# Kernel tuning notes

Hardware: AMD Instinct MI355X
Metric: run time of the kernel (lower is better)

The kernel has to match this reference:

```python
import jax, jax.numpy as jnp
import numpy as np

N_HEAD = 12
MIN_SIZE = 4
MAX_SIZE = 8
TOP_M = 16
ALPHA = 1.0
EPS = 1e-6
NEG_INF = -1e30


def setup_inputs() -> dict:
    key = jax.random.key(0)
    ks = jax.random.split(key, 4)
    B, T, C = 2, 512, 768
    x = jax.random.normal(ks[0], (B, T, C), jnp.float32)
    w_qkv = jax.random.normal(ks[1], (C, 3 * C), jnp.float32) * (1.0 / np.sqrt(C))
    b_qkv = jnp.zeros((3 * C,), jnp.float32)
    w_proj = jax.random.normal(ks[2], (C, C), jnp.float32) * (1.0 / np.sqrt(C))
    b_proj = jnp.zeros((C,), jnp.float32)
    gate_param = jnp.zeros((), jnp.float32)  # dpp_gate_init = 0.0 -> gate = 0.5
    return {"x": x, "w_qkv": w_qkv, "b_qkv": b_qkv, "w_proj": w_proj,
            "b_proj": b_proj, "gate_param": gate_param}


def _dpp_token(i, q_i, k, v):
    """Greedy DPP subset selection + attention for one query token.
    q_i: [hd], k/v: [T, hd]. Faithful to the torch greedy loop, vectorized
    over candidates with incremental Gram construction (scores only gate the
    discrete selection, so they are computed under stop_gradient, matching
    torch where they only feed Python comparisons)."""
    T, hd = k.shape
    kc = jax.lax.stop_gradient(k)
    qc = jax.lax.stop_gradient(q_i)
    # causal similarity, topk candidates
    sim = jnp.where(jnp.arange(T) <= i, kc @ qc, NEG_INF)
    _, topidx = jax.lax.top_k(sim, TOP_M)  # [M]
    # candidates = top-min(TOP_M, i+1) causal neighbors, excluding i itself
    cand_active = (jnp.arange(TOP_M) < jnp.minimum(TOP_M, i + 1)) & (topidx != i)
    cand_keys = kc[topidx]                              # [M, hd]
    cnorm = jnp.sum(cand_keys * cand_keys, axis=-1)     # [M]

    sel_idx = jnp.zeros((MAX_SIZE,), jnp.int32).at[0].set(i)
    sel_count = jnp.int32(1)
    # initial score: log(det([k_i.k_i]) + eps) / 1**alpha
    cur = jnp.log(jnp.dot(kc[i], kc[i]) + EPS)
    stopped = jnp.bool_(False)
    eye = jnp.eye(MAX_SIZE, dtype=jnp.float32)
    slots = jnp.arange(MAX_SIZE)

    for _ in range(MAX_SIZE - 1):
        rowmask = slots < sel_count                       # [S] current subset rows
        pos = (slots == sel_count).astype(jnp.float32)    # slot for new candidate
        Ksel = kc[sel_idx] * rowmask[:, None].astype(jnp.float32)  # [S, hd]
        G0 = Ksel @ Ksel.T                                # [S, S]
        cross = cand_keys @ Ksel.T                        # [M, S]
        # Gc[c,a,b] = G0[a,b] + pos[a]*cross[c,b] + pos[b]*cross[c,a] + pos[a]pos[b]*cnorm[c]
        Gc = (G0[None]
              + pos[None, :, None] * cross[:, None, :]
              + pos[None, None, :] * cross[:, :, None]
              + (pos[:, None] * pos[None, :])[None] * cnorm[:, None, None])
        newmask = rowmask | (slots == sel_count)
        # identity-pad unused rows/cols so det equals det of the active submatrix
        Gc = Gc + (eye * (1.0 - newmask.astype(jnp.float32)))[None]
        dets = jnp.linalg.det(Gc)                         # [M] (float32, as torch)
        size = (sel_count + 1).astype(jnp.float32)
        score = jnp.log(dets + EPS) / size ** ALPHA       # minimize_det=False
        masked = jnp.where(cand_active, score, NEG_INF)
        best = jnp.argmax(masked)
        best_score = masked[best]
        any_cand = jnp.any(cand_active)
        take = any_cand & (~stopped) & ((best_score > cur) | (sel_count < MIN_SIZE))
        sel_idx = jnp.where(take, sel_idx.at[sel_count].set(topidx[best].astype(jnp.int32)), sel_idx)
        cand_active = jnp.where(take, cand_active.at[best].set(False), cand_active)
        cur = jnp.where(take, best_score, cur)
        sel_count = sel_count + take.astype(jnp.int32)
        stopped = stopped | (~take)

    # attention over the selected subset (gradients flow through k, v, q here)
    rowmask = slots < sel_count
    Ks = k[sel_idx]
    Vs = v[sel_idx]
    logits = jnp.where(rowmask, (Ks @ q_i) / np.float32(np.sqrt(hd)), NEG_INF)
    w = jax.nn.softmax(logits)
    return w @ Vs


def _forward(x, w_qkv, b_qkv, w_proj, b_proj, gate_param):
    B, T, C = x.shape
    hd = C // N_HEAD
    qkv = x @ w_qkv + b_qkv
    q, k, v = jnp.split(qkv, 3, axis=-1)

    def heads(t):  # [B,T,C] -> [B*NH, T, hd]
        return t.reshape(B, T, N_HEAD, hd).transpose(0, 2, 1, 3).reshape(B * N_HEAD, T, hd)

    q, k, v = heads(q), heads(k), heads(v)

    # standard causal softmax attention (flash path, dropout=0 at eval)
    scale = np.float32(1.0 / np.sqrt(hd))
    att = jnp.einsum('nqd,nkd->nqk', q, k) * scale
    causal = jnp.tril(jnp.ones((T, T), bool))
    att = jnp.where(causal[None], att, NEG_INF)
    y_std = jnp.einsum('nqk,nkd->nqd', jax.nn.softmax(att, axis=-1), v)

    # DPP greedy-selection attention, vmapped over tokens and (batch*head)
    dpp_head = jax.vmap(_dpp_token, in_axes=(0, 0, None, None))
    y_dpp = jax.vmap(lambda qh, kh, vh: dpp_head(jnp.arange(T), qh, kh, vh))(q, k, v)

    gate = jax.nn.sigmoid(gate_param)
    y = gate * y_dpp + (1.0 - gate) * y_std
    y = y.reshape(B, N_HEAD, T, hd).transpose(0, 2, 1, 3).reshape(B, T, C)
    return y @ w_proj + b_proj


def reference(x, w_qkv, b_qkv, w_proj, b_proj, gate_param):
    return _forward(x, w_qkv, b_qkv, w_proj, b_proj, gate_param)
```

## Files before the change

kernel.cpp:

```cpp
#include <hip/hip_runtime.h>
#include <math.h>

constexpr int SEQ   = 512;
constexpr int HDIM  = 64;
constexpr int NHEAD = 12;
constexpr int NBATCH = 2;
constexpr int CDIM  = 768;
constexpr int TOPM  = 16;
constexpr int SMAX  = 8;
constexpr float NEGINF = -1e30f;

typedef short bf16x8 __attribute__((ext_vector_type(8)));
typedef float f32x4  __attribute__((ext_vector_type(4)));

__device__ inline void gload_lds16(const void* src, void* lds_base)
{
    __builtin_amdgcn_global_load_lds(
        (const __attribute__((address_space(1))) void*)src,
        (__attribute__((address_space(3))) void*)lds_base, 16, 0, 0);
}

__device__ inline unsigned short f2bf(float f)
{
    unsigned u = __float_as_uint(f);
    return (unsigned short)((u + 0x7FFFu + ((u >> 16) & 1u)) >> 16);
}
__device__ inline float bf2f(unsigned short h)
{
    return __uint_as_float((unsigned)h << 16);
}

__global__ __launch_bounds__(256) void split_x_kernel(
    const float* __restrict__ x, unsigned short* __restrict__ xh,
    unsigned short* __restrict__ xm, unsigned short* __restrict__ xl)
{
    const int idx = (blockIdx.x * 256 + threadIdx.x) * 4;
    float4 v = *(const float4*)(x + idx);
    float vv[4] = {v.x, v.y, v.z, v.w};
    unsigned short h[4], m[4], l[4];
    #pragma unroll
    for (int e = 0; e < 4; ++e) {
        float f = vv[e];
        unsigned short bh = f2bf(f);
        float r1 = f - bf2f(bh);
        unsigned short bm2 = f2bf(r1);
        float r2 = r1 - bf2f(bm2);
        h[e] = bh; m[e] = bm2; l[e] = f2bf(r2);
    }
    *(ushort4*)(xh + idx) = make_ushort4(h[0], h[1], h[2], h[3]);
    *(ushort4*)(xm + idx) = make_ushort4(m[0], m[1], m[2], m[3]);
    *(ushort4*)(xl + idx) = make_ushort4(l[0], l[1], l[2], l[3]);
}

__global__ __launch_bounds__(256) void tsplit_w_kernel(
    const float* __restrict__ w, unsigned short* __restrict__ wh,
    unsigned short* __restrict__ wm, unsigned short* __restrict__ wl)
{
    __shared__ float T[64][65];
    const int c0 = blockIdx.x * 64;
    const int k0 = blockIdx.y * 64;
    const int tid = threadIdx.x;
    #pragma unroll
    for (int i = 0; i < 16; ++i) {
        int idx = tid + i * 256;
        int kk = idx >> 6, cc = idx & 63;
        T[kk][cc] = w[(size_t)(k0 + kk) * (3 * CDIM) + c0 + cc];
    }
    __syncthreads();
    #pragma unroll
    for (int i = 0; i < 16; ++i) {
        int idx = tid + i * 256;
        int col = idx >> 6, kk = idx & 63;
        float f = T[kk][col];
        unsigned short bh = f2bf(f);
        float r1 = f - bf2f(bh);
        unsigned short bm2 = f2bf(r1);
        float r2 = r1 - bf2f(bm2);
        size_t o = (size_t)(c0 + col) * CDIM + k0 + kk;
        wh[o] = bh; wm[o] = bm2; wl[o] = f2bf(r2);
    }
}

__global__ __launch_bounds__(256) void qkv_mfma_kernel(
    const unsigned short* __restrict__ xh, const unsigned short* __restrict__ xm,
    const unsigned short* __restrict__ xl, const unsigned short* __restrict__ wh,
    const unsigned short* __restrict__ wm, const unsigned short* __restrict__ wl,
    const float* __restrict__ bias,
    float* __restrict__ q, float* __restrict__ k, float* __restrict__ v)
{
    __shared__ unsigned short As[3][64 * 32];
    __shared__ unsigned short Bs[3][64 * 32];
    const int bn = blockIdx.x * 64;
    const int bm = blockIdx.y * 64;
    const int tid = threadIdx.x;
    const int wid = tid >> 6;
    const int lane = tid & 63;
    const int lrow = lane & 15;
    const int lk8 = (lane >> 4) << 3;

    f32x4 acc[4];
    #pragma unroll
    for (int b = 0; b < 4; ++b) acc[b] = (f32x4){0.f, 0.f, 0.f, 0.f};

    const unsigned short* xs[3] = {xh, xm, xl};
    const unsigned short* wsrc[3] = {wh, wm, wl};

    const int slot = wid * 64 + lane;
    const int srow = slot >> 2;
    const int sk8 = (slot & 3) << 3;

    for (int k0 = 0; k0 < CDIM; k0 += 32) {
        #pragma unroll
        for (int c = 0; c < 3; ++c)
            gload_lds16(xs[c] + (size_t)(bm + srow) * CDIM + k0 + sk8,
                        &As[c][wid * 512]);
        #pragma unroll
        for (int c = 0; c < 3; ++c)
            gload_lds16(wsrc[c] + (size_t)(bn + srow) * CDIM + k0 + sk8,
                        &Bs[c][wid * 512]);
        __syncthreads();

        bf16x8 bf[3][4];
        #pragma unroll
        for (int c = 0; c < 3; ++c)
            #pragma unroll
            for (int ni = 0; ni < 4; ++ni)
                bf[c][ni] = *(const bf16x8*)&Bs[c][(ni * 16 + lrow) * 32 + lk8];

        bf16x8 ah = *(const bf16x8*)&As[0][(wid * 16 + lrow) * 32 + lk8];
        bf16x8 am = *(const bf16x8*)&As[1][(wid * 16 + lrow) * 32 + lk8];
        bf16x8 al = *(const bf16x8*)&As[2][(wid * 16 + lrow) * 32 + lk8];
        #pragma unroll
        for (int ni = 0; ni < 4; ++ni) {
            f32x4 a = acc[ni];
            a = __builtin_amdgcn_mfma_f32_16x16x32_bf16(al, bf[0][ni], a, 0, 0, 0);
            a = __builtin_amdgcn_mfma_f32_16x16x32_bf16(ah, bf[2][ni], a, 0, 0, 0);
            a = __builtin_amdgcn_mfma_f32_16x16x32_bf16(am, bf[1][ni], a, 0, 0, 0);
            a = __builtin_amdgcn_mfma_f32_16x16x32_bf16(am, bf[0][ni], a, 0, 0, 0);
            a = __builtin_amdgcn_mfma_f32_16x16x32_bf16(ah, bf[1][ni], a, 0, 0, 0);
            a = __builtin_amdgcn_mfma_f32_16x16x32_bf16(ah, bf[0][ni], a, 0, 0, 0);
            acc[ni] = a;
        }
        __syncthreads();
    }

    const int rbase = (lane >> 4) << 2;
    #pragma unroll
    for (int ni = 0; ni < 4; ++ni) {
        int cc = bn + ni * 16 + lrow;
        float bval = bias[cc];
        int part = cc / CDIM;
        int c2 = cc - part * CDIM;
        int hh = c2 >> 6, d = c2 & 63;
        float* dst = (part == 0) ? q : ((part == 1) ? k : v);
        #pragma unroll
        for (int r = 0; r < 4; ++r) {
            int m = bm + wid * 16 + rbase + r;
            int b_ = m >> 9, t = m & 511;
            dst[((((size_t)b_ * NHEAD + hh) * SEQ) + t) * HDIM + d] =
                acc[ni][r] + bval;
        }
    }
}

__global__ __launch_bounds__(256) void qkkt_kernel(
    const float* __restrict__ q, const float* __restrict__ k,
    float* __restrict__ S, float* __restrict__ KKT)
{
    __shared__ float Qs[64][68];
    __shared__ float Ka[64][68];
    __shared__ float Kb[64][68];
    const int e = blockIdx.x;
    const int n = blockIdx.y;
    int it = 0, start = 0;
    while (start + it + 1 <= e) { start += it + 1; ++it; }
    const int jt = e - start;
    const int tid = threadIdx.x;
    const float* qh = q + (size_t)n * SEQ * HDIM;
    const float* kh = k + (size_t)n * SEQ * HDIM;

    #pragma unroll
    for (int l = 0; l < 4; ++l) {
        int idx = tid + l * 256;
        int tok = idx >> 4, d4 = (idx & 15) << 2;
        *(float4*)&Qs[tok][d4] = *(const float4*)(qh + (it * 64 + tok) * HDIM + d4);
        *(float4*)&Ka[tok][d4] = *(const float4*)(kh + (it * 64 + tok) * HDIM + d4);
        *(float4*)&Kb[tok][d4] = *(const float4*)(kh + (jt * 64 + tok) * HDIM + d4);
    }
    __syncthreads();

    const int tm = (tid >> 4) << 2;
    const int tn = (tid & 15) << 2;
    float sacc[4][4] = {};
    float gacc[4][4] = {};
    #pragma unroll 4
    for (int d4 = 0; d4 < 16; ++d4) {
        float4 qr[4], ar[4], br[4];
        #pragma unroll
        for (int u = 0; u < 4; ++u) {
            qr[u] = *(const float4*)&Qs[tm + u][d4 << 2];
            ar[u] = *(const float4*)&Ka[tm + u][d4 << 2];
        }
        #pragma unroll
        for (int w2 = 0; w2 < 4; ++w2)
            br[w2] = *(const float4*)&Kb[tn + w2][d4 << 2];
        #pragma unroll
        for (int u = 0; u < 4; ++u)
            #pragma unroll
            for (int w2 = 0; w2 < 4; ++w2) {
                float s = sacc[u][w2];
                s = fmaf(qr[u].x, br[w2].x, s);
                s = fmaf(qr[u].y, br[w2].y, s);
                s = fmaf(qr[u].z, br[w2].z, s);
                s = fmaf(qr[u].w, br[w2].w, s);
                sacc[u][w2] = s;
                float g = gacc[u][w2];
                g = fmaf(ar[u].x, br[w2].x, g);
                g = fmaf(ar[u].y, br[w2].y, g);
                g = fmaf(ar[u].z, br[w2].z, g);
                g = fmaf(ar[u].w, br[w2].w, g);
                gacc[u][w2] = g;
            }
    }
    float* gdst = KKT + ((size_t)n * 36 + e) * 4096;
    #pragma unroll
    for (int u = 0; u < 4; ++u) {
        int i = it * 64 + tm + u;
        float4 o = {sacc[u][0], sacc[u][1], sacc[u][2], sacc[u][3]};
        *(float4*)(S + ((size_t)n * SEQ + i) * SEQ + jt * 64 + tn) = o;
        float4 g = {gacc[u][0], gacc[u][1], gacc[u][2], gacc[u][3]};
        *(float4*)(gdst + (tm + u) * 64 + tn) = g;
    }
}

__device__ inline double hybrid_log(double a)
{
    unsigned long long b = __double_as_longlong(a);
    int e2 = (int)((b >> 52) & 0x7FF) - 1022;
    double m = __longlong_as_double((b & 0x000FFFFFFFFFFFFFULL) |
                                    0x3FE0000000000000ULL);
    return ((double)__log2f((float)m) + (double)e2) * 0.6931471805599453;
}

__device__ inline double rsqrt64(double x)
{
    double r = (double)rsqrtf((float)x);
    r = r * (1.5 - 0.5 * x * r * r);
    return r;
}

#define CSW(a, b)                                                        \
    {                                                                    \
        bool sw = (v##a < v##b) || ((v##a == v##b) && (j##a > j##b));    \
        float tf = sw ? v##b : v##a;                                     \
        float uf = sw ? v##a : v##b;                                     \
        int ti = sw ? j##b : j##a;                                       \
        int ui = sw ? j##a : j##b;                                       \
        v##a = tf; v##b = uf; j##a = ti; j##b = ui;                      \
    }

__global__ __launch_bounds__(128) void dpp_kernel(
    const float* __restrict__ v, float* __restrict__ S,
    const float* __restrict__ KKT, const float* __restrict__ gate_p,
    float* __restrict__ y, float* __restrict__ denomArr)
{
    const int tid  = threadIdx.x;
    const int wid  = tid >> 6;
    const int lane = tid & 63;
    const int i = blockIdx.x * 2 + wid;
    const int n = blockIdx.y;
    const float* vh = v + (size_t)n * SEQ * HDIM;
    const float* KKTh = KKT + (size_t)n * 36 * 4096;
    float* Srow = S + ((size_t)n * SEQ + i) * SEQ;

    __shared__ float prow[2][SEQ];
    __shared__ float gramf[2][17][17];
    __shared__ int   eidx[2][17];
    __shared__ int   selS[2][SMAX];

    float sim8[8];
    #pragma unroll
    for (int m = 0; m < 8; ++m) {
        int j = lane + (m << 6);
        sim8[m] = (j <= i) ? Srow[j] : NEGINF;
    }
    if (lane < SMAX) selS[wid][lane] = i;

    {
        float v0 = sim8[0], v1 = sim8[1], v2 = sim8[2], v3 = sim8[3],
              v4 = sim8[4], v5 = sim8[5], v6 = sim8[6], v7 = sim8[7];
        int j0 = lane, j1 = lane + 64, j2 = lane + 128, j3 = lane + 192,
            j4 = lane + 256, j5 = lane + 320, j6 = lane + 384, j7 = lane + 448;
        CSW(0, 1) CSW(2, 3) CSW(4, 5) CSW(6, 7)
        CSW(0, 2) CSW(1, 3) CSW(4, 6) CSW(5, 7)
        CSW(1, 2) CSW(5, 6)
        CSW(0, 4) CSW(1, 5) CSW(2, 6) CSW(3, 7)
        CSW(2, 4) CSW(3, 5)
        CSW(1, 2) CSW(3, 4) CSW(5, 6)

        if (lane == 0) eidx[wid][0] = i;
        #pragma unroll
        for (int s = 0; s < TOPM; ++s) {
            float rv = v0;
            #pragma unroll
            for (int off = 32; off; off >>= 1)
                rv = fmaxf(rv, __shfl_xor(rv, off));
            unsigned long long tied = __ballot(v0 == rv);
            int ri;
            if (__popcll(tied) == 1) {
                ri = __shfl(j0, (int)__builtin_ctzll(tied));
            } else {
                int cnd = (v0 == rv) ? j0 : 0x7FFFFFFF;
                #pragma unroll
                for (int off = 32; off; off >>= 1)
                    cnd = min(cnd, __shfl_xor(cnd, off));
                ri = cnd;
            }
            if (lane == 0) eidx[wid][1 + s] = ri;
            if (v0 == rv && j0 == ri) {
                v0 = v1; j0 = j1; v1 = v2; j1 = j2; v2 = v3; j2 = j3;
                v3 = v4; j3 = j4; v4 = v5; j4 = j5; v5 = v6; j5 = j6;
                v6 = v7; j6 = j7; v7 = -3e38f; j7 = 1023;
            }
        }
    }

    const float scale = 0.125f;
    float lm = -3e38f;
    #pragma unroll
    for (int m = 0; m < 8; ++m) lm = fmaxf(lm, sim8[m]);
    #pragma unroll
    for (int off = 32; off; off >>= 1) lm = fmaxf(lm, __shfl_xor(lm, off));
    const float mx = lm * scale;
    float sum = 0.f;
    #pragma unroll
    for (int m = 0; m < 8; ++m) {
        float p = expf(sim8[m] * scale - mx);
        int j = lane + (m << 6);
        prow[wid][j] = p;
        Srow[j] = p;
        sum += p;
    }
    #pragma unroll
    for (int off = 32; off; off >>= 1) sum += __shfl_xor(sum, off);
    const float denom = sum;
    asm volatile("s_waitcnt lgkmcnt(0)" ::: "memory");

    for (int e = lane; e < 153; e += 64) {
        int a = (int)((sqrtf(8.f * (float)e + 1.f) - 1.f) * 0.5f);
        int st = (a * (a + 1)) >> 1;
        if (st > e) { --a; st = (a * (a + 1)) >> 1; }
        else if (st + a + 1 <= e) { ++a; st = (a * (a + 1)) >> 1; }
        int b = e - st;
        int ra = eidx[wid][a], rb = eidx[wid][b];
        int row = ra > rb ? ra : rb;
        int col = ra > rb ? rb : ra;
        int itt = row >> 6, jtt = col >> 6;
        int p = ((itt * (itt + 1)) >> 1) + jtt;
        float s = KKTh[((size_t)p * 64 + (row & 63)) * 64 + (col & 63)];
        gramf[wid][a][b] = s;
        gramf[wid][b][a] = s;
    }
    asm volatile("s_waitcnt lgkmcnt(0)" ::: "memory");

    int sc = 1;
    {
        const int c = lane;
        const bool isCand = (c < TOPM);
        const int nvalid = (i + 1 < TOPM) ? (i + 1) : TOPM;
        bool active = isCand && (c < nvalid) && (eidx[wid][1 + c] != i);
        double zc[7];
        #pragma unroll
        for (int t = 0; t < 7; ++t) zc[t] = 0.0;
        double det = (double)gramf[wid][0][0];
        double cur = 0.0;
        double invL00 = rsqrt64(det > 0.0 ? det : 1e-30);
        double dcv = 0.0;
        if (isCand) {
            zc[0] = (double)gramf[wid][1 + c][0] * invL00;
            dcv = (double)gramf[wid][1 + c][1 + c] - zc[0] * zc[0];
        }

        for (int it2 = 0; it2 < SMAX - 1; ++it2) {
            double argc = det * dcv + 1e-6;
            double key = active ? (argc > 0.0 ? argc : 1e300) : -1.0;
            int rc = c;
            #pragma unroll
            for (int off = 1; off <= 8; off <<= 1) {
                double ov = __shfl_xor(key, off);
                int    oc = __shfl_xor(rc, off);
                if (ov > key || (ov == key && oc < rc)) { key = ov; rc = oc; }
            }
            rc = __shfl(rc, 0);
            bool any = (__any(active ? 1 : 0) != 0);
            double dbest = __shfl(dcv, rc);
            bool take;
            if (it2 < 2) {
                take = any;
            } else {
                double argb = det * dbest + 1e-6;
                bool pos = argb > 0.0;
                double score = hybrid_log(pos ? argb : 1.0) / (double)(sc + 1);
                take = any && (it2 < 3 || (pos && score > cur));
                if (take) cur = pos ? score : __builtin_nan("");
            }
            if (!take) break;

            double invLss = rsqrt64(dbest > 1e-30 ? dbest : 1e-30);
            double zb[7];
            #pragma unroll
            for (int t = 0; t < 7; ++t) zb[t] = __shfl(zc[t], rc);
            if (isCand) {
                double crossn = (double)gramf[wid][1 + c][1 + rc];
                double s2 = 0.0;
                #pragma unroll
                for (int t = 0; t < 7; ++t) s2 += zc[t] * zb[t];
                double znew = (crossn - s2) * invLss;
                #pragma unroll
                for (int t = 0; t < 7; ++t) if (t == sc) zc[t] = znew;
                dcv -= znew * znew;
            }
            det = det * dbest;
            if (c == rc) active = false;
            if (lane == 0) selS[wid][sc] = eidx[wid][1 + rc];
            ++sc;
        }
    }

    int selI[SMAX];
    #pragma unroll
    for (int s = 0; s < SMAX; ++s) selI[s] = selS[wid][s];
    float wsum = 0.f;
    #pragma unroll
    for (int s = 0; s < SMAX; ++s) if (s < sc) wsum += prow[wid][selI[s]];
    float yd = 0.f;
    #pragma unroll
    for (int s = 0; s < SMAX; ++s)
        if (s < sc) yd = fmaf(prow[wid][selI[s]], vh[selI[s] * HDIM + lane], yd);
    const float gp = gate_p[0];
    const float gate = 1.f / (1.f + expf(-gp));
    y[((size_t)n * SEQ + i) * HDIM + lane] = gate * yd / wsum;
    if (lane == 0) denomArr[n * SEQ + i] = denom;
}

__global__ __launch_bounds__(256) void pv_gemm_kernel(
    const float* __restrict__ P, const float* __restrict__ v,
    const float* __restrict__ denomArr, const float* __restrict__ gate_p,
    float* __restrict__ y)
{
    __shared__ float Ps[32][36];
    __shared__ float Vs[32][68];
    const int tt = blockIdx.x;
    const int n  = blockIdx.y;
    const int t0 = tt * 32;
    const int tid = threadIdx.x;
    const float* Ph = P + (size_t)n * SEQ * SEQ;
    const float* vh = v + (size_t)n * SEQ * HDIM;
    const int tm = (tid >> 4) << 1;
    const int tn = (tid & 15) << 2;
    float acc[2][4] = {};
    const int jmax = t0 + 32;
    for (int j0 = 0; j0 < jmax; j0 += 32) {
        {
            int tok = tid >> 3, j4 = (tid & 7) << 2;
            *(float4*)&Ps[tok][j4] =
                *(const float4*)(Ph + (t0 + tok) * SEQ + j0 + j4);
        }
        #pragma unroll
        for (int l = 0; l < 2; ++l) {
            int idx = tid + l * 256;
            int j = idx >> 4, d4 = (idx & 15) << 2;
            *(float4*)&Vs[j][d4] = *(const float4*)(vh + (j0 + j) * HDIM + d4);
        }
        __syncthreads();
        #pragma unroll
        for (int j4 = 0; j4 < 8; ++j4) {
            float4 p0r = *(const float4*)&Ps[tm + 0][j4 << 2];
            float4 p1r = *(const float4*)&Ps[tm + 1][j4 << 2];
            float pr[2][4] = {{p0r.x, p0r.y, p0r.z, p0r.w},
                              {p1r.x, p1r.y, p1r.z, p1r.w}};
            #pragma unroll
            for (int l = 0; l < 4; ++l) {
                float4 v4 = *(const float4*)&Vs[(j4 << 2) + l][tn];
                float vv[4] = {v4.x, v4.y, v4.z, v4.w};
                #pragma unroll
                for (int u = 0; u < 2; ++u)
                    #pragma unroll
                    for (int w2 = 0; w2 < 4; ++w2)
                        acc[u][w2] = fmaf(pr[u][l], vv[w2], acc[u][w2]);
            }
        }
        __syncthreads();
    }
    const float gp = gate_p[0];
    const float gate = 1.f / (1.f + expf(-gp));
    #pragma unroll
    for (int u = 0; u < 2; ++u) {
        int i = t0 + tm + u;
        float den = denomArr[n * SEQ + i];
        #pragma unroll
        for (int w2 = 0; w2 < 4; ++w2) {
            int d = tn + w2;
            size_t off = ((size_t)n * SEQ + i) * HDIM + d;
            y[off] += (1.f - gate) * acc[u][w2] / den;
        }
    }
}

__global__ __launch_bounds__(256) void proj_gemm_kernel(
    const float* __restrict__ y, const float* __restrict__ w,
    float* __restrict__ partial)
{
    __shared__ float As[128][36];
    __shared__ float Bs[32][68];
    const int bm = blockIdx.y * 128;
    const int bn = blockIdx.x * 64;
    const int kbase = blockIdx.z * 96;
    const int tid = threadIdx.x;
    const int tm = (tid >> 4) << 3;
    const int tn = (tid & 15) << 2;
    const int blk = tid >> 3;
    const int bln = (tid & 7) << 3;

    float acc[8][4] = {};
    for (int t = 0; t < 3; ++t) {
        const int k0 = kbase + t * 32;
        float4 av[4];
        #pragma unroll
        for (int l = 0; l < 4; ++l) {
            int idx = tid + l * 256;
            int row = bm + (idx >> 3);
            int col = k0 + ((idx & 7) << 2);
            int b_ = row >> 9, tk = row & 511;
            int h = col >> 6, d = col & 63;
            av[l] = *(const float4*)(y + ((((size_t)b_ * NHEAD + h) * SEQ) + tk) * HDIM + d);
        }
        float4 b0 = *(const float4*)(w + (k0 + blk) * CDIM + bn + bln);
        float4 b1 = *(const float4*)(w + (k0 + blk) * CDIM + bn + bln + 4);
        #pragma unroll
        for (int l = 0; l < 4; ++l) {
            int idx = tid + l * 256;
            int row = idx >> 3, kq = (idx & 7) << 2;
            *(float4*)&As[row][kq] = av[l];
        }
        *(float4*)&Bs[blk][bln] = b0;
        *(float4*)&Bs[blk][bln + 4] = b1;
        __syncthreads();
        #pragma unroll
        for (int k4 = 0; k4 < 8; ++k4) {
            float ar[8][4];
            #pragma unroll
            for (int u = 0; u < 8; ++u) {
                float4 a4 = *(const float4*)&As[tm + u][k4 << 2];
                ar[u][0] = a4.x; ar[u][1] = a4.y;
                ar[u][2] = a4.z; ar[u][3] = a4.w;
            }
            #pragma unroll
            for (int j = 0; j < 4; ++j) {
                float4 b4 = *(const float4*)&Bs[(k4 << 2) + j][tn];
                float bb[4] = {b4.x, b4.y, b4.z, b4.w};
                #pragma unroll
                for (int u = 0; u < 8; ++u)
                    #pragma unroll
                    for (int w2 = 0; w2 < 4; ++w2)
                        acc[u][w2] = fmaf(ar[u][j], bb[w2], acc[u][w2]);
            }
        }
        __syncthreads();
    }
    float* dst = partial + (size_t)blockIdx.z * (1024 * 768);
    #pragma unroll
    for (int u = 0; u < 8; ++u) {
        float4 o = {acc[u][0], acc[u][1], acc[u][2], acc[u][3]};
        *(float4*)(dst + (size_t)(bm + tm + u) * 768 + bn + tn) = o;
    }
}

__global__ __launch_bounds__(256) void proj_reduce_kernel(
    const float* __restrict__ partial, const float* __restrict__ bias,
    float* __restrict__ out)
{
    const int idx = blockIdx.x * 256 + threadIdx.x;
    const int m = idx / 192;
    const int cc = (idx - m * 192) << 2;
    const size_t MN = (size_t)1024 * 768;
    float4 s = *(const float4*)(partial + (size_t)m * 768 + cc);
    #pragma unroll
    for (int z = 1; z < 8; ++z) {
        float4 p = *(const float4*)(partial + (size_t)z * MN + (size_t)m * 768 + cc);
        s.x += p.x; s.y += p.y; s.z += p.z; s.w += p.w;
    }
    float4 b4 = *(const float4*)(bias + cc);
    float4 o = {s.x + b4.x, s.y + b4.y, s.z + b4.z, s.w + b4.w};
    *(float4*)(out + (size_t)m * 768 + cc) = o;
}

extern "C" void kernel_launch(void* const* d_in, const int* in_sizes, int n_in,
                              void* d_out, int out_size, void* d_ws, size_t ws_size,
                              hipStream_t stream)
{
    const float* x      = (const float*)d_in[0];
    const float* w_qkv  = (const float*)d_in[1];
    const float* b_qkv  = (const float*)d_in[2];
    const float* w_proj = (const float*)d_in[3];
    const float* b_proj = (const float*)d_in[4];
    const float* gate_p = (const float*)d_in[5];
    float* out = (float*)d_out;

    float* ws = (float*)d_ws;
    const size_t HS = (size_t)NBATCH * NHEAD * SEQ * HDIM;
    const size_t SS = (size_t)NBATCH * NHEAD * SEQ * SEQ;
    float* q   = ws;
    float* k   = q + HS;
    float* v   = k + HS;
    float* y   = v + HS;
    float* S   = y + HS;
    float* den = S + SS;
    float* KKT = den + 16384;

    unsigned short* us = (unsigned short*)S;
    unsigned short* xh = us;
    unsigned short* xm = us + 786432;
    unsigned short* xl = us + 1572864;
    unsigned short* wh = us + 2359296;
    unsigned short* wm = us + 2359296 + 1769472;
    unsigned short* wl = us + 2359296 + 3538944;

    split_x_kernel<<<768, 256, 0, stream>>>(x, xh, xm, xl);
    tsplit_w_kernel<<<dim3(36, 12), 256, 0, stream>>>(w_qkv, wh, wm, wl);
    qkv_mfma_kernel<<<dim3(36, 16), 256, 0, stream>>>(
        xh, xm, xl, wh, wm, wl, b_qkv, q, k, v);
    qkkt_kernel<<<dim3(36, NBATCH * NHEAD), 256, 0, stream>>>(q, k, S, KKT);
    dpp_kernel<<<dim3(SEQ / 2, NBATCH * NHEAD), 128, 0, stream>>>(
        v, S, KKT, gate_p, y, den);
    pv_gemm_kernel<<<dim3(SEQ / 32, NBATCH * NHEAD), 256, 0, stream>>>(
        S, v, den, gate_p, y);
    proj_gemm_kernel<<<dim3(CDIM / 64, (NBATCH * SEQ) / 128, 8), 256, 0, stream>>>(
        y, w_proj, S);
    proj_reduce_kernel<<<768, 256, 0, stream>>>(S, b_proj, out);
}
```

Before: 169.8 us.

## Compute QK^T and KK^T tiles with split-bf16 MFMA instead of FP32 FMAs

Replaces the scalar FP32 FMA tile kernel for the causal Q·K and K·K Gram tiles with an MFMA kernel. Each fp32 operand is split into three bf16 parts and six bf16 MFMAs are accumulated to emulate fp32 precision. Tiles are staged into LDS with direct global-to-LDS loads. It also factors the three-way bf16 split into a shared helper. The gain from matrix cores is offset by split overhead in registers and scattered scalar output stores, and the six-term emulation may differ slightly from true fp32, which matters for the discrete top-k selection.

After: 164.0 us (median of 2 runs). 1.04x faster.

```diff
diff --git a/kernel.cpp b/kernel.cpp
--- a/kernel.cpp
+++ b/kernel.cpp
@@ -29,6 +29,14 @@
 {
     return __uint_as_float((unsigned)h << 16);
 }
+__device__ inline void split3(float f, unsigned short& h,
+                              unsigned short& m, unsigned short& l)
+{
+    h = f2bf(f);
+    float r1 = f - bf2f(h);
+    m = f2bf(r1);
+    l = f2bf(r1 - bf2f(m));
+}
 
 __global__ __launch_bounds__(256) void split_x_kernel(
     const float* __restrict__ x, unsigned short* __restrict__ xh,
@@ -39,14 +47,7 @@
     float vv[4] = {v.x, v.y, v.z, v.w};
     unsigned short h[4], m[4], l[4];
     #pragma unroll
-    for (int e = 0; e < 4; ++e) {
-        float f = vv[e];
-        unsigned short bh = f2bf(f);
-        float r1 = f - bf2f(bh);
-        unsigned short bm2 = f2bf(r1);
-        float r2 = r1 - bf2f(bm2);
-        h[e] = bh; m[e] = bm2; l[e] = f2bf(r2);
-    }
+    for (int e = 0; e < 4; ++e) split3(vv[e], h[e], m[e], l[e]);
     *(ushort4*)(xh + idx) = make_ushort4(h[0], h[1], h[2], h[3]);
     *(ushort4*)(xm + idx) = make_ushort4(m[0], m[1], m[2], m[3]);
     *(ushort4*)(xl + idx) = make_ushort4(l[0], l[1], l[2], l[3]);
@@ -71,13 +72,10 @@
     for (int i = 0; i < 16; ++i) {
         int idx = tid + i * 256;
         int col = idx >> 6, kk = idx & 63;
-        float f = T[kk][col];
-        unsigned short bh = f2bf(f);
-        float r1 = f - bf2f(bh);
-        unsigned short bm2 = f2bf(r1);
-        float r2 = r1 - bf2f(bm2);
+        unsigned short h, m, l;
+        split3(T[kk][col], h, m, l);
         size_t o = (size_t)(c0 + col) * CDIM + k0 + kk;
-        wh[o] = bh; wm[o] = bm2; wl[o] = f2bf(r2);
+        wh[o] = h; wm[o] = m; wl[o] = l;
     }
 }
 
@@ -163,73 +161,108 @@
     }
 }
 
-__global__ __launch_bounds__(256) void qkkt_kernel(
+__global__ __launch_bounds__(256) void qkkt_mfma_kernel(
     const float* __restrict__ q, const float* __restrict__ k,
     float* __restrict__ S, float* __restrict__ KKT)
 {
-    __shared__ float Qs[64][68];
-    __shared__ float Ka[64][68];
-    __shared__ float Kb[64][68];
+    __shared__ float Qs[64 * 32];
+    __shared__ float Kas[64 * 32];
+    __shared__ float Kbs[64 * 32];
     const int e = blockIdx.x;
     const int n = blockIdx.y;
     int it = 0, start = 0;
     while (start + it + 1 <= e) { start += it + 1; ++it; }
     const int jt = e - start;
     const int tid = threadIdx.x;
+    const int wid = tid >> 6;
+    const int lane = tid & 63;
+    const int lrow = lane & 15;
+    const int lk8 = (lane >> 4) << 3;
     const float* qh = q + (size_t)n * SEQ * HDIM;
     const float* kh = k + (size_t)n * SEQ * HDIM;
 
-    #pragma unroll
-    for (int l = 0; l < 4; ++l) {
-        int idx = tid + l * 256;
-        int tok = idx >> 4, d4 = (idx & 15) << 2;
-        *(float4*)&Qs[tok][d4] = *(const float4*)(qh + (it * 64 + tok) * HDIM + d4);
-        *(float4*)&Ka[tok][d4] = *(const float4*)(kh + (it * 64 + tok) * HDIM + d4);
-        *(float4*)&Kb[tok][d4] = *(const float4*)(kh + (jt * 64 + tok) * HDIM + d4);
-    }
-    __syncthreads();
-
-    const int tm = (tid >> 4) << 2;
-    const int tn = (tid & 15) << 2;
-    float sacc[4][4] = {};
-    float gacc[4][4] = {};
-    #pragma unroll 4
-    for (int d4 = 0; d4 < 16; ++d4) {
-        float4 qr[4], ar[4], br[4];
-        #pragma unroll
-        for (int u = 0; u < 4; ++u) {
-            qr[u] = *(const float4*)&Qs[tm + u][d4 << 2];
-            ar[u] = *(const float4*)&Ka[tm + u][d4 << 2];
-        }
-        #pragma unroll
-        for (int w2 = 0; w2 < 4; ++w2)
-            br[w2] = *(const float4*)&Kb[tn + w2][d4 << 2];
-        #pragma unroll
-        for (int u = 0; u < 4; ++u)
-            #pragma unroll
-            for (int w2 = 0; w2 < 4; ++w2) {
-                float s = sacc[u][w2];
-                s = fmaf(qr[u].x, br[w2].x, s);
-                s = fmaf(qr[u].y, br[w2].y, s);
-                s = fmaf(qr[u].z, br[w2].z, s);
-                s = fmaf(qr[u].w, br[w2].w, s);
-                sacc[u][w2] = s;
-                float g = gacc[u][w2];
-                g = fmaf(ar[u].x, br[w2].x, g);
-                g = fmaf(ar[u].y, br[w2].y, g);
-                g = fmaf(ar[u].z, br[w2].z, g);
-                g = fmaf(ar[u].w, br[w2].w, g);
-                gacc[u][w2] = g;
-            }
-    }
+    f32x4 accS[4], accG[4];
+    #pragma unroll
+    for (int b = 0; b < 4; ++b) {
+        accS[b] = (f32x4){0.f, 0.f, 0.f, 0.f};
+        accG[b] = (f32x4){0.f, 0.f, 0.f, 0.f};
+    }
+
+    #pragma unroll
+    for (int ks = 0; ks < 2; ++ks) {
+        const int k0 = ks * 32;
+        #pragma unroll
+        for (int l = 0; l < 2; ++l) {
+            int g = l * 256 + wid * 64 + lane;
+            int r = g >> 3, f4 = (g & 7) << 2;
+            float* dstQ = Qs + (l * 256 + wid * 64) * 4;
+            float* dstA = Kas + (l * 256 + wid * 64) * 4;
+            float* dstB = Kbs + (l * 256 + wid * 64) * 4;
+            gload_lds16(qh + (size_t)(it * 64 + r) * HDIM + k0 + f4, dstQ);
+            gload_lds16(kh + (size_t)(it * 64 + r) * HDIM + k0 + f4, dstA);
+            gload_lds16(kh + (size_t)(jt * 64 + r) * HDIM + k0 + f4, dstB);
+        }
+        __syncthreads();
+
+        bf16x8 qfh, qfm, qfl, afh, afm, afl;
+        {
+            const float* qr = Qs + (wid * 16 + lrow) * 32 + lk8;
+            const float* ar = Kas + (wid * 16 + lrow) * 32 + lk8;
+            #pragma unroll
+            for (int e2 = 0; e2 < 8; ++e2) {
+                unsigned short h, m, l;
+                split3(qr[e2], h, m, l);
+                qfh[e2] = (short)h; qfm[e2] = (short)m; qfl[e2] = (short)l;
+                split3(ar[e2], h, m, l);
+                afh[e2] = (short)h; afm[e2] = (short)m; afl[e2] = (short)l;
+            }
+        }
+        bf16x8 bfh[4], bfm[4], bfl[4];
+        #pragma unroll
+        for (int ni = 0; ni < 4; ++ni) {
+            const float* br = Kbs + (ni * 16 + lrow) * 32 + lk8;
+            #pragma unroll
+            for (int e2 = 0; e2 < 8; ++e2) {
+                unsigned short h, m, l;
+                split3(br[e2], h, m, l);
+                bfh[ni][e2] = (short)h; bfm[ni][e2] = (short)m; bfl[ni][e2] = (short)l;
+            }
+        }
+        #pragma unroll
+        for (int ni = 0; ni < 4; ++ni) {
+            f32x4 a = accS[ni];
+            a = __builtin_amdgcn_mfma_f32_16x16x32_bf16(qfl, bfh[ni], a, 0, 0, 0);
+            a = __builtin_amdgcn_mfma_f32_16x16x32_bf16(qfh, bfl[ni], a, 0, 0, 0);
+            a = __builtin_amdgcn_mfma_f32_16x16x32_bf16(qfm, bfm[ni], a, 0, 0, 0);
+            a = __builtin_amdgcn_mfma_f32_16x16x32_bf16(qfm, bfh[ni], a, 0, 0, 0);
+            a = __builtin_amdgcn_mfma_f32_16x16x32_bf16(qfh, bfm[ni], a, 0, 0, 0);
+            a = __builtin_amdgcn_mfma_f32_16x16x32_bf16(qfh, bfh[ni], a, 0, 0, 0);
+            accS[ni] = a;
+            f32x4 g = accG[ni];
+            g = __builtin_amdgcn_mfma_f32_16x16x32_bf16(afl, bfh[ni], g, 0, 0, 0);
+            g = __builtin_amdgcn_mfma_f32_16x16x32_bf16(afh, bfl[ni], g, 0, 0, 0);
+            g = __builtin_amdgcn_mfma_f32_16x16x32_bf16(afm, bfm[ni], g, 0, 0, 0);
+            g = __builtin_amdgcn_mfma_f32_16x16x32_bf16(afm, bfh[ni], g, 0, 0, 0);
+            g = __builtin_amdgcn_mfma_f32_16x16x32_bf16(afh, bfm[ni], g, 0, 0, 0);
+            g = __builtin_amdgcn_mfma_f32_16x16x32_bf16(afh, bfh[ni], g, 0, 0, 0);
+            accG[ni] = g;
+        }
+        __syncthreads();
+    }
+
+    const int rbase = (lane >> 4) << 2;
     float* gdst = KKT + ((size_t)n * 36 + e) * 4096;
     #pragma unroll
-    for (int u = 0; u < 4; ++u) {
-        int i = it * 64 + tm + u;
-        float4 o = {sacc[u][0], sacc[u][1], sacc[u][2], sacc[u][3]};
-        *(float4*)(S + ((size_t)n * SEQ + i) * SEQ + jt * 64 + tn) = o;
-        float4 g = {gacc[u][0], gacc[u][1], gacc[u][2], gacc[u][3]};
-        *(float4*)(gdst + (tm + u) * 64 + tn) = g;
+    for (int ni = 0; ni < 4; ++ni) {
+        int coll = ni * 16 + lrow;
+        int col = jt * 64 + coll;
+        #pragma unroll
+        for (int r = 0; r < 4; ++r) {
+            int rowl = wid * 16 + rbase + r;
+            int row = it * 64 + rowl;
+            S[((size_t)n * SEQ + row) * SEQ + col] = accS[ni][r];
+            gdst[rowl * 64 + coll] = accG[ni][r];
+        }
     }
 }
 
@@ -630,7 +663,7 @@
     tsplit_w_kernel<<<dim3(36, 12), 256, 0, stream>>>(w_qkv, wh, wm, wl);
     qkv_mfma_kernel<<<dim3(36, 16), 256, 0, stream>>>(
         xh, xm, xl, wh, wm, wl, b_qkv, q, k, v);
-    qkkt_kernel<<<dim3(36, NBATCH * NHEAD), 256, 0, stream>>>(q, k, S, KKT);
+    qkkt_mfma_kernel<<<dim3(36, NBATCH * NHEAD), 256, 0, stream>>>(q, k, S, KKT);
     dpp_kernel<<<dim3(SEQ / 2, NBATCH * NHEAD), 128, 0, stream>>>(
         v, S, KKT, gate_p, y, den);
     pv_gemm_kernel<<<dim3(SEQ / 32, NBATCH * NHEAD), 256, 0, stream>>>(
```
